# Performance work log

Hardware: AMD Instinct MI355X
Metric: run time of the kernel (lower is better)

The kernel has to match this reference:

```python
import jax, jax.numpy as jnp
import numpy as np

B, T, I, H, L = 256, 512, 64, 256, 2


def _lstm_layer(x, Wih, Whh, bih, bhh):
    # x: [B, T, Din]; Wih: [4H, Din]; Whh: [4H, H]; gate order i,f,g,o (PyTorch)
    Hdim = Whh.shape[1]
    # Precompute input projections for all timesteps (one big GEMM)
    x_proj = jnp.einsum('btd,gd->btg', x, Wih) + bih + bhh  # [B, T, 4H]
    x_proj = jnp.transpose(x_proj, (1, 0, 2))  # [T, B, 4H]

    def step(carry, xt):
        h, c = carry
        gates = xt + h @ Whh.T  # [B, 4H]
        i, f, g, o = jnp.split(gates, 4, axis=-1)
        i = jax.nn.sigmoid(i)
        f = jax.nn.sigmoid(f)
        g = jnp.tanh(g)
        o = jax.nn.sigmoid(o)
        c = f * c + i * g
        h = o * jnp.tanh(c)
        return (h, c), h

    b = x.shape[0]
    h0 = jnp.zeros((b, Hdim), dtype=x.dtype)
    c0 = jnp.zeros((b, Hdim), dtype=x.dtype)
    _, hs = jax.lax.scan(step, (h0, c0), x_proj)  # hs: [T, B, H]
    return jnp.transpose(hs, (1, 0, 2))  # [B, T, H]


def setup_inputs() -> dict:
    key = jax.random.key(0)
    ks = jax.random.split(key, 12)
    s_in = 1.0 / np.sqrt(H)
    inp = {
        'x': jax.random.normal(ks[0], (B, T, I), dtype=jnp.float32),
        'Wih0': jax.random.uniform(ks[1], (4 * H, I), minval=-s_in, maxval=s_in),
        'Whh0': jax.random.uniform(ks[2], (4 * H, H), minval=-s_in, maxval=s_in),
        'bih0': jax.random.uniform(ks[3], (4 * H,), minval=-s_in, maxval=s_in),
        'bhh0': jax.random.uniform(ks[4], (4 * H,), minval=-s_in, maxval=s_in),
        'Wih1': jax.random.uniform(ks[5], (4 * H, H), minval=-s_in, maxval=s_in),
        'Whh1': jax.random.uniform(ks[6], (4 * H, H), minval=-s_in, maxval=s_in),
        'bih1': jax.random.uniform(ks[7], (4 * H,), minval=-s_in, maxval=s_in),
        'bhh1': jax.random.uniform(ks[8], (4 * H,), minval=-s_in, maxval=s_in),
        'Wfc': jax.random.uniform(ks[9], (1, H), minval=-s_in, maxval=s_in),
        'bfc': jax.random.uniform(ks[10], (1,), minval=-s_in, maxval=s_in),
    }
    return inp


def reference(x, Wih0, Whh0, bih0, bhh0, Wih1, Whh1, bih1, bhh1, Wfc, bfc):
    h1 = _lstm_layer(x, Wih0, Whh0, bih0, bhh0)   # [B, T, H]
    h2 = _lstm_layer(h1, Wih1, Whh1, bih1, bhh1)  # [B, T, H]
    last = h2[:, -1, :]                           # [B, H]
    return last @ Wfc.T + bfc                     # [B, 1]
```

## Files before the change

kernel.cpp:

```cpp
#include <hip/hip_runtime.h>

#define TT   512
#define IDIM 64
#define HDIM 256

typedef short  short8  __attribute__((ext_vector_type(8)));
typedef short  short4v __attribute__((ext_vector_type(4)));
typedef float  f32x4   __attribute__((ext_vector_type(4)));
typedef unsigned long long u64;

__device__ __forceinline__ short f2bf(float f) {
    unsigned u = __float_as_uint(f);
    u = u + 0x7FFFu + ((u >> 16) & 1u);
    return (short)(u >> 16);
}
__device__ __forceinline__ float bf2f(short h) {
    return __uint_as_float(((unsigned)(unsigned short)h) << 16);
}
__device__ __forceinline__ float sigm(float x)  { return 1.0f / (1.0f + __expf(-x)); }
__device__ __forceinline__ float tanh_(float x) { return 2.0f / (1.0f + __expf(-2.0f * x)) - 1.0f; }

__device__ __forceinline__ void unpack16(const u64 W[6], u64 q[4]) {
    unsigned short u[16];
#pragma unroll
    for (int w = 0; w < 6; ++w)
#pragma unroll
        for (int k = 0; k < 3; ++k) {
            int j = 3 * w + k;
            if (j < 16) u[j] = (unsigned short)(W[w] >> (16 * k));
        }
#pragma unroll
    for (int t = 0; t < 4; ++t)
        q[t] = (u64)u[4*t] | ((u64)u[4*t+1] << 16) | ((u64)u[4*t+2] << 32) | ((u64)u[4*t+3] << 48);
}

__global__ __launch_bounds__(256, 1) void lstm_fused(
    const float* __restrict__ x,
    const float* __restrict__ Wih0, const float* __restrict__ Whh0,
    const float* __restrict__ bih0, const float* __restrict__ bhh0,
    const float* __restrict__ Wih1, const float* __restrict__ Whh1,
    const float* __restrict__ bih1, const float* __restrict__ bhh1,
    const float* __restrict__ Wfc,  const float* __restrict__ bfc,
    float* __restrict__ out, char* __restrict__ ws)
{
    u64* h0buf = (u64*)ws;
    u64* h1buf = h0buf + 2 * 16 * 16 * 96;

    const int blk   = blockIdx.x;
    const int grp   = ((blk & 7) << 1) | ((blk >> 3) & 1);
    const int chunk = blk >> 4;
    const int tid   = threadIdx.x;
    const int lane  = tid & 63;
    const int wave  = tid >> 6;
    const int quad  = lane >> 4;
    const int nn    = lane & 15;

    __shared__ short A0[16][328];
    __shared__ short A1[16][520];
    __shared__ float gbuf[2][4][16][17];
    __shared__ float red[16][16];
    __shared__ float ldspad[5120];

    for (int i = tid; i < 16 * 328; i += 256) (&A0[0][0])[i] = 0;
    for (int i = tid; i < 16 * 520; i += 256) (&A1[0][0])[i] = 0;

    const int wrow = wave * HDIM + chunk * 16 + nn;
    short8 w0f[10];
    short8 w1f[16];
#pragma unroll
    for (int kb = 0; kb < 10; ++kb)
#pragma unroll
        for (int j = 0; j < 8; ++j) {
            int k = kb * 32 + quad * 8 + j;
            float v = (k < 64) ? Wih0[wrow * IDIM + k] : Whh0[wrow * HDIM + (k - 64)];
            w0f[kb][j] = f2bf(v);
        }
#pragma unroll
    for (int kb = 0; kb < 16; ++kb)
#pragma unroll
        for (int j = 0; j < 8; ++j) {
            int k = kb * 32 + quad * 8 + j;
            float v = (k < 256) ? Wih1[wrow * HDIM + k] : Whh1[wrow * HDIM + (k - 256)];
            w1f[kb][j] = f2bf(v);
        }
    const float bias0 = bih0[wrow] + bhh0[wrow];
    const float bias1 = bih1[wrow] + bhh1[wrow];

    const int em = tid >> 4;
    const int ej = tid & 15;
    float c0 = 0.0f, c1 = 0.0f;

    auto load_x = [&](int t) {
        const float4 v = *(const float4*)&x[((size_t)(grp * 16 + em) * TT + t) * IDIM + ej * 4];
        short4v sv;
        sv[0] = f2bf(v.x); sv[1] = f2bf(v.y); sv[2] = f2bf(v.z); sv[3] = f2bf(v.w);
        *(short4v*)&A0[em][ej * 4] = sv;
    };

    __syncthreads();
    load_x(0);
    __syncthreads();

    for (int s = 0; s <= TT; ++s) {
        if (s < TT) {
            f32x4 accA = {0.f, 0.f, 0.f, 0.f}, accB = {0.f, 0.f, 0.f, 0.f};
#pragma unroll
            for (int kb = 0; kb < 10; kb += 2) {
                short8 a0v = *(const short8*)&A0[nn][kb * 32 + quad * 8];
                short8 a1v = *(const short8*)&A0[nn][(kb + 1) * 32 + quad * 8];
                accA = __builtin_amdgcn_mfma_f32_16x16x32_bf16(a0v, w0f[kb],     accA, 0, 0, 0);
                accB = __builtin_amdgcn_mfma_f32_16x16x32_bf16(a1v, w0f[kb + 1], accB, 0, 0, 0);
            }
            const f32x4 acc = accA + accB;
#pragma unroll
            for (int r = 0; r < 4; ++r)
                gbuf[0][wave][quad * 4 + r][nn] = acc[r] + bias0;
        }
        __syncthreads();

        {
            const bool gh1 = (s >= 2);
            const unsigned sq1 = (unsigned)s;
            const size_t rb1 = (((size_t)((s - 1) & 1) * 16 + grp) * 16 + em) * 96 + ej * 6;
            u64 W1[6];
            if (gh1) {
#pragma unroll
                for (int i = 0; i < 6; ++i)
                    W1[i] = __hip_atomic_load(&h1buf[rb1 + i],
                                              __ATOMIC_RELAXED, __HIP_MEMORY_SCOPE_AGENT);
            }

            if (s < TT) {
                float gi = sigm (gbuf[0][0][em][ej]);
                float gf = sigm (gbuf[0][1][em][ej]);
                float gg = tanh_(gbuf[0][2][em][ej]);
                float go = sigm (gbuf[0][3][em][ej]);
                c0 = gf * c0 + gi * gg;
                const short h0v = f2bf(go * tanh_(c0));
                const int hv = (int)(unsigned short)h0v;
                const int n1 = __shfl_down(hv, 1);
                const int n2 = __shfl_down(hv, 2);
                if ((ej % 3) == 0) {
                    const int w = ej / 3;
                    u64 v0 = (u64)(unsigned)(s + 1) << 48;
                    v0 |= (u64)(unsigned)hv;
                    if (w < 5) {
                        v0 |= (u64)(unsigned)n1 << 16;
                        v0 |= (u64)(unsigned)n2 << 32;
                    }
                    const size_t base = (((size_t)(s & 1) * 16 + grp) * 16 + em) * 96
                                        + chunk * 6 + w;
                    (void)__hip_atomic_exchange(&h0buf[base], v0,
                                                __ATOMIC_RELAXED, __HIP_MEMORY_SCOPE_AGENT);
                }
            }

            if (gh1) {
                bool ok = true;
#pragma unroll
                for (int i = 0; i < 6; ++i) ok &= ((unsigned)(W1[i] >> 48) == sq1);
                int budget = 1 << 17;
                while (!ok && budget-- > 0) {
#pragma unroll
                    for (int i = 0; i < 6; ++i)
                        W1[i] = __hip_atomic_load(&h1buf[rb1 + i],
                                                  __ATOMIC_RELAXED, __HIP_MEMORY_SCOPE_AGENT);
                    ok = true;
#pragma unroll
                    for (int i = 0; i < 6; ++i) ok &= ((unsigned)(W1[i] >> 48) == sq1);
                }
                u64 q[4]; unpack16(W1, q);
                u64* d2 = (u64*)&A1[em][256 + ej * 16];
#pragma unroll
                for (int t = 0; t < 4; ++t) d2[t] = q[t];
            }
        }
        __syncthreads();

        if (s >= 1) {
            f32x4 accA = {0.f, 0.f, 0.f, 0.f}, accB = {0.f, 0.f, 0.f, 0.f};
#pragma unroll
            for (int kb = 0; kb < 16; kb += 2) {
                short8 a0v = *(const short8*)&A1[nn][kb * 32 + quad * 8];
                short8 a1v = *(const short8*)&A1[nn][(kb + 1) * 32 + quad * 8];
                accA = __builtin_amdgcn_mfma_f32_16x16x32_bf16(a0v, w1f[kb],     accA, 0, 0, 0);
                accB = __builtin_amdgcn_mfma_f32_16x16x32_bf16(a1v, w1f[kb + 1], accB, 0, 0, 0);
            }
            const f32x4 acc = accA + accB;
#pragma unroll
            for (int r = 0; r < 4; ++r)
                gbuf[1][wave][quad * 4 + r][nn] = acc[r] + bias1;
        }
        __syncthreads();

        {
            short h1v = 0;
            if (s >= 1) {
                float gi = sigm (gbuf[1][0][em][ej]);
                float gf = sigm (gbuf[1][1][em][ej]);
                float gg = tanh_(gbuf[1][2][em][ej]);
                float go = sigm (gbuf[1][3][em][ej]);
                c1 = gf * c1 + gi * gg;
                h1v = f2bf(go * tanh_(c1));
            }
            const int hv = (int)(unsigned short)h1v;
            const int n1 = __shfl_down(hv, 1);
            const int n2 = __shfl_down(hv, 2);
            if ((ej % 3) == 0) {
                const int w = ej / 3;
                u64 v1 = (u64)(unsigned)(s + 1) << 48;
                v1 |= (u64)(unsigned)hv;
                if (w < 5) {
                    v1 |= (u64)(unsigned)n1 << 16;
                    v1 |= (u64)(unsigned)n2 << 32;
                }
                const size_t base = (((size_t)(s & 1) * 16 + grp) * 16 + em) * 96
                                    + chunk * 6 + w;
                (void)__hip_atomic_exchange(&h1buf[base], v1,
                                            __ATOMIC_RELAXED, __HIP_MEMORY_SCOPE_AGENT);
            }
        }

        if (s + 1 < TT) load_x(s + 1);

        {
            const bool g0 = (s < TT);
            const unsigned sq = (unsigned)(s + 1);
            const size_t rb = (((size_t)(s & 1) * 16 + grp) * 16 + em) * 96 + ej * 6;
            if (g0) {
                u64 W0[6];
                bool ok0 = false;
                int budget = 1 << 17;
                do {
#pragma unroll
                    for (int i = 0; i < 6; ++i)
                        W0[i] = __hip_atomic_load(&h0buf[rb + i],
                                                  __ATOMIC_RELAXED, __HIP_MEMORY_SCOPE_AGENT);
                    ok0 = true;
#pragma unroll
                    for (int i = 0; i < 6; ++i) ok0 &= ((unsigned)(W0[i] >> 48) == sq);
                } while (!ok0 && budget-- > 0);

                u64 q[4]; unpack16(W0, q);
                u64* d0 = (u64*)&A0[em][64 + ej * 16];
                u64* d1 = (u64*)&A1[em][ej * 16];
#pragma unroll
                for (int t = 0; t < 4; ++t) { d0[t] = q[t]; d1[t] = q[t]; }
            }
            asm volatile("s_waitcnt vmcnt(0)" ::: "memory");
        }
        __syncthreads();
    }

    {
        const unsigned sq = (unsigned)(TT + 1);
        const size_t rb = (((size_t)(TT & 1) * 16 + grp) * 16 + em) * 96 + ej * 6;
        u64 W1[6];
        bool ok = false;
        int budget = 1 << 17;
        do {
#pragma unroll
            for (int i = 0; i < 6; ++i)
                W1[i] = __hip_atomic_load(&h1buf[rb + i],
                                          __ATOMIC_RELAXED, __HIP_MEMORY_SCOPE_AGENT);
            ok = true;
#pragma unroll
            for (int i = 0; i < 6; ++i) ok &= ((unsigned)(W1[i] >> 48) == sq);
        } while (!ok && budget-- > 0);
        u64 q[4]; unpack16(W1, q);
        u64* d2 = (u64*)&A1[em][256 + ej * 16];
#pragma unroll
        for (int t = 0; t < 4; ++t) d2[t] = q[t];
    }
    __syncthreads();

    {
        float part = 0.f;
#pragma unroll
        for (int kk = 0; kk < 16; ++kk) {
            int k = ej * 16 + kk;
            part += bf2f(A1[em][256 + k]) * Wfc[k];
        }
        red[em][ej] = part;
    }
    __syncthreads();
    if (chunk == 0 && tid < 16) {
        float sum = bfc[0];
#pragma unroll
        for (int c = 0; c < 16; ++c) sum += red[tid][c];
        out[grp * 16 + tid] = sum;
    }

    if (gridDim.x > 100000) { ldspad[tid] = bias0; out[0] = ldspad[255 - tid]; }
}

extern "C" void kernel_launch(void* const* d_in, const int* in_sizes, int n_in,
                              void* d_out, int out_size, void* d_ws, size_t ws_size,
                              hipStream_t stream) {
    (void)in_sizes; (void)n_in; (void)out_size; (void)ws_size;
    const float* x    = (const float*)d_in[0];
    const float* Wih0 = (const float*)d_in[1];
    const float* Whh0 = (const float*)d_in[2];
    const float* bih0 = (const float*)d_in[3];
    const float* bhh0 = (const float*)d_in[4];
    const float* Wih1 = (const float*)d_in[5];
    const float* Whh1 = (const float*)d_in[6];
    const float* bih1 = (const float*)d_in[7];
    const float* bhh1 = (const float*)d_in[8];
    const float* Wfc  = (const float*)d_in[9];
    const float* bfc  = (const float*)d_in[10];

    lstm_fused<<<256, 256, 0, stream>>>(x, Wih0, Whh0, bih0, bhh0,
                                        Wih1, Whh1, bih1, bhh1, Wfc, bfc,
                                        (float*)d_out, (char*)d_ws);
}
```

Baseline: 1.622 ms.

## Split layer-0 hidden exchange into data words plus per-chunk tag flag

```diff
diff --git a/kernel.cpp b/kernel.cpp
--- a/kernel.cpp
+++ b/kernel.cpp
@@ -43,8 +43,9 @@
     const float* __restrict__ Wfc,  const float* __restrict__ bfc,
     float* __restrict__ out, char* __restrict__ ws)
 {
-    u64* h0buf = (u64*)ws;
-    u64* h1buf = h0buf + 2 * 16 * 16 * 96;
+    u64* h0dat = (u64*)ws;
+    u64* h0tag = h0dat + 2 * 16 * 16 * 64;
+    u64* h1buf = h0tag + 2 * 16 * 16 * 16;
 
     const int blk   = blockIdx.x;
     const int grp   = ((blk & 7) << 1) | ((blk >> 3) & 1);
@@ -140,19 +141,23 @@
                 const int hv = (int)(unsigned short)h0v;
                 const int n1 = __shfl_down(hv, 1);
                 const int n2 = __shfl_down(hv, 2);
-                if ((ej % 3) == 0) {
-                    const int w = ej / 3;
-                    u64 v0 = (u64)(unsigned)(s + 1) << 48;
-                    v0 |= (u64)(unsigned)hv;
-                    if (w < 5) {
-                        v0 |= (u64)(unsigned)n1 << 16;
-                        v0 |= (u64)(unsigned)n2 << 32;
-                    }
-                    const size_t base = (((size_t)(s & 1) * 16 + grp) * 16 + em) * 96
-                                        + chunk * 6 + w;
-                    (void)__hip_atomic_exchange(&h0buf[base], v0,
+                const int n3 = __shfl_down(hv, 3);
+                if ((ej & 3) == 0) {
+                    u64 d = (u64)(unsigned)(hv & 0xFFFF)
+                          | ((u64)(unsigned)(n1 & 0xFFFF) << 16)
+                          | ((u64)(unsigned)(n2 & 0xFFFF) << 32)
+                          | ((u64)(unsigned)(n3 & 0xFFFF) << 48);
+                    const size_t di = (((size_t)(s & 1) * 16 + grp) * 16 + em) * 64
+                                      + chunk * 4 + (ej >> 2);
+                    (void)__hip_atomic_exchange(&h0dat[di], d,
                                                 __ATOMIC_RELAXED, __HIP_MEMORY_SCOPE_AGENT);
                 }
+            }
+            asm volatile("s_waitcnt vmcnt(0)" ::: "memory");
+            if (s < TT && ej == 0) {
+                const size_t ti = (((size_t)(s & 1) * 16 + grp) * 16 + em) * 16 + chunk;
+                (void)__hip_atomic_exchange(&h0tag[ti], (u64)(unsigned)(s + 1),
+                                            __ATOMIC_RELAXED, __HIP_MEMORY_SCOPE_AGENT);
             }
 
             if (gh1) {
@@ -209,10 +214,10 @@
             if ((ej % 3) == 0) {
                 const int w = ej / 3;
                 u64 v1 = (u64)(unsigned)(s + 1) << 48;
-                v1 |= (u64)(unsigned)hv;
+                v1 |= (u64)(unsigned)(hv & 0xFFFF);
                 if (w < 5) {
-                    v1 |= (u64)(unsigned)n1 << 16;
-                    v1 |= (u64)(unsigned)n2 << 32;
+                    v1 |= (u64)(unsigned)(n1 & 0xFFFF) << 16;
+                    v1 |= (u64)(unsigned)(n2 & 0xFFFF) << 32;
                 }
                 const size_t base = (((size_t)(s & 1) * 16 + grp) * 16 + em) * 96
                                     + chunk * 6 + w;
@@ -225,27 +230,30 @@
 
         {
             const bool g0 = (s < TT);
-            const unsigned sq = (unsigned)(s + 1);
-            const size_t rb = (((size_t)(s & 1) * 16 + grp) * 16 + em) * 96 + ej * 6;
             if (g0) {
-                u64 W0[6];
-                bool ok0 = false;
+                const u64 sq = (u64)(unsigned)(s + 1);
+                const size_t ti = (((size_t)(s & 1) * 16 + grp) * 16 + em) * 16 + ej;
+                u64 t;
                 int budget = 1 << 17;
                 do {
-#pragma unroll
-                    for (int i = 0; i < 6; ++i)
-                        W0[i] = __hip_atomic_load(&h0buf[rb + i],
-                                                  __ATOMIC_RELAXED, __HIP_MEMORY_SCOPE_AGENT);
-                    ok0 = true;
-#pragma unroll
-                    for (int i = 0; i < 6; ++i) ok0 &= ((unsigned)(W0[i] >> 48) == sq);
-                } while (!ok0 && budget-- > 0);
-
-                u64 q[4]; unpack16(W0, q);
+                    t = __hip_atomic_load(&h0tag[ti],
+                                          __ATOMIC_RELAXED, __HIP_MEMORY_SCOPE_AGENT);
+                } while (t != sq && budget-- > 0);
+                asm volatile("" ::: "memory");
+
+                const size_t di = (((size_t)(s & 1) * 16 + grp) * 16 + em) * 64 + ej * 4;
+                const u64 q0 = __hip_atomic_load(&h0dat[di + 0],
+                                                 __ATOMIC_RELAXED, __HIP_MEMORY_SCOPE_AGENT);
+                const u64 q1 = __hip_atomic_load(&h0dat[di + 1],
+                                                 __ATOMIC_RELAXED, __HIP_MEMORY_SCOPE_AGENT);
+                const u64 q2 = __hip_atomic_load(&h0dat[di + 2],
+                                                 __ATOMIC_RELAXED, __HIP_MEMORY_SCOPE_AGENT);
+                const u64 q3 = __hip_atomic_load(&h0dat[di + 3],
+                                                 __ATOMIC_RELAXED, __HIP_MEMORY_SCOPE_AGENT);
                 u64* d0 = (u64*)&A0[em][64 + ej * 16];
                 u64* d1 = (u64*)&A1[em][ej * 16];
-#pragma unroll
-                for (int t = 0; t < 4; ++t) { d0[t] = q[t]; d1[t] = q[t]; }
+                d0[0] = q0; d0[1] = q1; d0[2] = q2; d0[3] = q3;
+                d1[0] = q0; d1[1] = q1; d1[2] = q2; d1[3] = q3;
             }
             asm volatile("s_waitcnt vmcnt(0)" ::: "memory");
         }
```

Result: slower. 1.870 ms (+15.3%).
